# Kernel optimization log

Hardware: AMD Instinct MI355X
Metric: run time of the kernel (lower is better)

## Reference

```python
import jax, jax.numpy as jnp
import numpy as np

N, E = 50000, 800000
IN, HID, OUT = 256, 128, 128


def setup_inputs() -> dict:
    key = jax.random.key(0)
    ks = jax.random.split(key, 6)
    x = jax.random.normal(ks[0], (N, IN), dtype=jnp.float32)
    edge_index = jax.random.randint(ks[1], (2, E), 0, N, dtype=jnp.int32)
    # xavier_normal-ish scales (exact init values irrelevant for correctness baseline)
    W1 = jax.random.normal(ks[2], (IN, HID), dtype=jnp.float32) * (1.414 / np.sqrt(IN))
    att_src = jax.random.normal(ks[3], (HID,), dtype=jnp.float32) * 0.1
    att_dst = jax.random.normal(ks[4], (HID,), dtype=jnp.float32) * 0.1
    W2 = jax.random.normal(ks[5], (HID, OUT), dtype=jnp.float32) * (1.414 / np.sqrt(HID))
    return {"x": x, "edge_index": edge_index, "W1": W1,
            "att_src": att_src, "att_dst": att_dst, "W2": W2}


def _gat_layer(x, edge_index, W, a_src, a_dst):
    """GATConv(heads=1, concat=False, add_self_loops=False, dropout=0), attention=True."""
    n = x.shape[0]
    src, dst = edge_index[0], edge_index[1]  # message x_j = h[src], grouped by index = dst
    h = x @ W                                 # (N, C)
    e_src = h @ a_src                         # (N,) per-node attention logits
    e_dst = h @ a_dst                         # (N,)
    # per-edge: sigmoid(alpha_j + alpha_i), then scatter-softmax over dst neighborhoods
    alpha = jax.nn.sigmoid(e_src[src] + e_dst[dst])             # (E,)
    m = jax.ops.segment_max(alpha, dst, num_segments=n)          # stable softmax max
    ex = jnp.exp(alpha - m[dst])
    denom = jax.ops.segment_sum(ex, dst, num_segments=n)
    w = ex / denom[dst]                                          # (E,)
    # scatter-add aggregation of weighted source features; heads=1 so mean over heads is identity
    return jax.ops.segment_sum(h[src] * w[:, None], dst, num_segments=n)  # (N, C)


def reference(x, edge_index, W1, att_src, att_dst, W2):
    h1 = jax.nn.elu(_gat_layer(x, edge_index, W1, att_src, att_dst))
    # conv2 called with attention=False: mm(h1, W2).view(N,1,C).mean(1) == plain linear
    return h1 @ W2
```

## Files before the change

kernel.cpp:

```cpp
#include <hip/hip_runtime.h>
#include <hip/hip_bf16.h>

#define N_NODES 50000
#define N_EDGES 800000
#define DIN 256
#define DHID 128
#define DOUT 128
#define NBUCK 196
#define BINBLK 256
#define EPB 3125
#define BINIT 13
#define G1BLK ((N_NODES + 63) / 64)

typedef __attribute__((ext_vector_type(8))) short bf16x8;
typedef __attribute__((ext_vector_type(4))) float f32x4;

__device__ inline unsigned short f2b(float f) {
    __hip_bfloat16 b = __float2bfloat16(f);
    return *reinterpret_cast<unsigned short*>(&b);
}

__global__ __launch_bounds__(256) void convW_lhist_kernel(
    const float* __restrict__ W1, const float* __restrict__ W2,
    const int* __restrict__ ei,
    unsigned short* __restrict__ W1t, unsigned short* __restrict__ W2t,
    int* __restrict__ blockHist)
{
    __shared__ int h[NBUCK];
    const int blk = blockIdx.x;
    const int tid = threadIdx.x;

    if (blk < 192) {
        int i = blk * 256 + tid;
        if (i < DIN * DHID) {
            int n = i >> 8, k = i & 255;
            int kt = k >> 5, q = (k >> 3) & 3, e = k & 7;
            int t = n >> 4, m = n & 15;
            W1t[(((kt * 8 + t) * 64) + (q * 16 + m)) * 8 + e] = f2b(W1[k * DHID + n]);
        } else {
            int j = i - DIN * DHID;
            int n = j >> 7, k = j & 127;
            int kt = k >> 5, q = (k >> 3) & 3, e = k & 7;
            int t = n >> 4, m = n & 15;
            W2t[(((kt * 8 + t) * 64) + (q * 16 + m)) * 8 + e] = f2b(W2[k * DOUT + n]);
        }
        return;
    }

    const int b = blk - 192;
    if (tid < NBUCK) h[tid] = 0;
    __syncthreads();
    const int base = b * EPB;
    #pragma unroll 1
    for (int it = 0; it < BINIT; ++it) {
        int e = base + it * 256 + tid;
        if (e < base + EPB)
            atomicAdd(&h[ei[N_EDGES + e] >> 8], 1);
    }
    __syncthreads();
    if (tid < NBUCK) blockHist[tid * 256 + b] = h[tid];
}

__global__ __launch_bounds__(256) void gemm1_scan_kernel(
    const float* __restrict__ x,
    const unsigned short* __restrict__ W1t,
    const float* __restrict__ att_src,
    const float* __restrict__ att_dst,
    const int* __restrict__ blockHist,
    unsigned short* __restrict__ hb,
    float* __restrict__ es,
    float* __restrict__ ed,
    int* __restrict__ matrixScan)
{
    __shared__ unsigned short W1s[DHID * DIN];

    const int tid = threadIdx.x;

    if (blockIdx.x >= G1BLK) {
        int* bs = (int*)W1s;
        int* s  = bs + 256;
        const int b = blockIdx.x - G1BLK;

        int tot = 0;
        if (tid < NBUCK) {
            const int* row = blockHist + tid * 256;
            #pragma unroll 4
            for (int i = 0; i < 256; ++i) tot += row[i];
        }
        bs[tid] = tot;
        __syncthreads();
        #pragma unroll
        for (int off = 1; off < 256; off <<= 1) {
            int u = (tid >= off) ? bs[tid - off] : 0;
            __syncthreads();
            bs[tid] += u;
            __syncthreads();
        }
        const int base = (b == 0) ? 0 : bs[b - 1];

        int c = blockHist[b * 256 + tid];
        s[tid] = c;
        __syncthreads();
        #pragma unroll
        for (int off = 1; off < 256; off <<= 1) {
            int u = (tid >= off) ? s[tid - off] : 0;
            __syncthreads();
            s[tid] += u;
            __syncthreads();
        }
        matrixScan[b * 256 + tid] = base + s[tid] - c;
        return;
    }

    const int wave = tid >> 6, lane = tid & 63;
    const int row0 = blockIdx.x * 64 + wave * 16;
    const int m = lane & 15, q = lane >> 4;

    {
        const float4* src = (const float4*)W1t;
        float4* dst = (float4*)W1s;
        #pragma unroll
        for (int i = 0; i < 16; ++i)
            dst[tid + i * 256] = src[tid + i * 256];
    }
    __syncthreads();

    int r  = row0 + m;
    int rc = (r < N_NODES) ? r : 0;

    f32x4 acc[8];
    #pragma unroll
    for (int t = 0; t < 8; ++t) acc[t] = (f32x4){0.f, 0.f, 0.f, 0.f};

    const float* xr = x + (size_t)rc * DIN + q * 8;
    const short* wfrag = (const short*)W1s + lane * 8;

    #pragma unroll
    for (int kt = 0; kt < 8; ++kt) {
        float4 f0 = *(const float4*)(xr + kt * 32);
        float4 f1 = *(const float4*)(xr + kt * 32 + 4);
        bf16x8 a;
        a[0] = (short)f2b(f0.x); a[1] = (short)f2b(f0.y);
        a[2] = (short)f2b(f0.z); a[3] = (short)f2b(f0.w);
        a[4] = (short)f2b(f1.x); a[5] = (short)f2b(f1.y);
        a[6] = (short)f2b(f1.z); a[7] = (short)f2b(f1.w);
        #pragma unroll
        for (int t = 0; t < 8; ++t) {
            bf16x8 b = *(const bf16x8*)(wfrag + (kt * 8 + t) * 512);
            acc[t] = __builtin_amdgcn_mfma_f32_16x16x32_bf16(a, b, acc[t], 0, 0, 0);
        }
    }

    #pragma unroll
    for (int reg = 0; reg < 4; ++reg) {
        int rr = row0 + q * 4 + reg;
        if (rr < N_NODES) {
            #pragma unroll
            for (int t = 0; t < 8; ++t)
                hb[(size_t)rr * DHID + t * 16 + m] = f2b(acc[t][reg]);
        }
    }

    float esr[4] = {0.f, 0.f, 0.f, 0.f}, edr[4] = {0.f, 0.f, 0.f, 0.f};
    #pragma unroll
    for (int t = 0; t < 8; ++t) {
        float as = att_src[t * 16 + m];
        float ad = att_dst[t * 16 + m];
        #pragma unroll
        for (int reg = 0; reg < 4; ++reg) {
            esr[reg] += acc[t][reg] * as;
            edr[reg] += acc[t][reg] * ad;
        }
    }
    #pragma unroll
    for (int off = 8; off; off >>= 1)
        #pragma unroll
        for (int reg = 0; reg < 4; ++reg) {
            esr[reg] += __shfl_xor(esr[reg], off);
            edr[reg] += __shfl_xor(edr[reg], off);
        }
    if (m == 0) {
        #pragma unroll
        for (int reg = 0; reg < 4; ++reg) {
            int rr = row0 + q * 4 + reg;
            if (rr < N_NODES) { es[rr] = esr[reg]; ed[rr] = edr[reg]; }
        }
    }
}

__global__ __launch_bounds__(256) void binpass_kernel(
    const int* __restrict__ ei,
    const float* __restrict__ es,
    const float* __restrict__ ed,
    const int* __restrict__ matrixScan,
    int2* __restrict__ binned)
{
    __shared__ int lcur[NBUCK];
    const int t = threadIdx.x, blk = blockIdx.x;
    if (t < NBUCK) lcur[t] = matrixScan[t * 256 + blk];
    __syncthreads();
    const int base = blk * EPB;
    #pragma unroll 1
    for (int it = 0; it < BINIT; ++it) {
        int e = base + it * 256 + t;
        if (e < base + EPB) {
            int s = ei[e];
            int d = ei[N_EDGES + e];
            float a  = es[s] + ed[d];
            float sg = 1.f / (1.f + __expf(-a));
            float w  = __expf(sg);
            int pos = atomicAdd(&lcur[d >> 8], 1);
            binned[pos] = make_int2(s | ((d & 255) << 16), __float_as_int(w));
        }
    }
}

__global__ __launch_bounds__(256) void sortpass_kernel(
    const int2* __restrict__ binned,
    const int* __restrict__ matrixScan,
    int2* __restrict__ sortedSW,
    int* __restrict__ offset,
    int* __restrict__ count)
{
    __shared__ int lhist[256], lscan[256], lcur[256];
    const int t = threadIdx.x, b = blockIdx.x;
    const int start = matrixScan[b * 256];
    const int end   = (b == NBUCK - 1) ? N_EDGES : matrixScan[(b + 1) * 256];
    const int cnt   = end - start;

    lhist[t] = 0;
    __syncthreads();
    for (int i = t; i < cnt; i += 256)
        atomicAdd(&lhist[(binned[start + i].x >> 16) & 255], 1);
    __syncthreads();

    int v = lhist[t];
    lscan[t] = v;
    __syncthreads();
    #pragma unroll
    for (int off = 1; off < 256; off <<= 1) {
        int u = (t >= off) ? lscan[t - off] : 0;
        __syncthreads();
        lscan[t] += u;
        __syncthreads();
    }
    int excl = lscan[t] - v;

    int node = (b << 8) + t;
    if (node < N_NODES) { offset[node] = start + excl; count[node] = v; }
    lcur[t] = excl;
    __syncthreads();

    for (int i = t; i < cnt; i += 256) {
        int2 ent = binned[start + i];
        int dlow = (ent.x >> 16) & 255;
        int pos = atomicAdd(&lcur[dlow], 1);
        sortedSW[start + pos] = make_int2(ent.x & 0xFFFF, ent.y);
    }
}

__global__ __launch_bounds__(256) void agg_kernel(
    const int2* __restrict__ sortedSW,
    const int* __restrict__ offset,
    const int* __restrict__ count,
    const unsigned short* __restrict__ hb,
    unsigned int* __restrict__ h1b)
{
    int node = (blockIdx.x * 256 + threadIdx.x) >> 6;
    int lane = threadIdx.x & 63;
    if (node >= N_NODES) return;

    int beg = offset[node];
    int deg = count[node];

    float2 acc = make_float2(0.f, 0.f);
    float wsum = 0.f;

    for (int base = 0; base < deg; base += 64) {
        int cnt = min(64, deg - base);
        int2 sw = (lane < cnt) ? sortedSW[beg + base + lane] : make_int2(0, 0);
        int j = 0;

#define TIER(T)                                                                 \
        for (; j + T <= cnt; j += T) {                                          \
            unsigned uu[T]; float ww[T];                                        \
            _Pragma("unroll")                                                   \
            for (int k = 0; k < T; ++k) {                                       \
                int s_ = __builtin_amdgcn_readlane(sw.x, j + k);                \
                uu[k] = *(const unsigned*)(hb + (size_t)s_ * DHID + 2 * lane);  \
            }                                                                   \
            _Pragma("unroll")                                                   \
            for (int k = 0; k < T; ++k)                                         \
                ww[k] = __uint_as_float(                                        \
                    (unsigned)__builtin_amdgcn_readlane(sw.y, j + k));          \
            _Pragma("unroll")                                                   \
            for (int k = 0; k < T; ++k) {                                       \
                wsum  += ww[k];                                                 \
                acc.x += ww[k] * __uint_as_float(uu[k] << 16);                  \
                acc.y += ww[k] * __uint_as_float(uu[k] & 0xffff0000u);          \
            }                                                                   \
        }

        TIER(16)
        TIER(8)
        TIER(4)
#undef TIER
        for (; j < cnt; ++j) {
            int   sj = __builtin_amdgcn_readlane(sw.x, j);
            float wj = __uint_as_float((unsigned)__builtin_amdgcn_readlane(sw.y, j));
            unsigned u = *(const unsigned*)(hb + (size_t)sj * DHID + 2 * lane);
            acc.x += wj * __uint_as_float(u << 16);
            acc.y += wj * __uint_as_float(u & 0xffff0000u);
            wsum  += wj;
        }
    }
    float inv = (deg > 0) ? 1.f / wsum : 0.f;
    float v0 = acc.x * inv, v1 = acc.y * inv;
    float e0 = v0 > 0.f ? v0 : (__expf(v0) - 1.f);
    float e1 = v1 > 0.f ? v1 : (__expf(v1) - 1.f);
    h1b[(size_t)node * (DHID / 2) + lane] =
        (unsigned)f2b(e0) | ((unsigned)f2b(e1) << 16);
}

__global__ __launch_bounds__(256) void gemm2_mfma(
    const unsigned short* __restrict__ h1b,
    const unsigned short* __restrict__ W2t,
    float* __restrict__ out)
{
    __shared__ unsigned short W2s[DOUT * DHID];

    const int tid = threadIdx.x;
    const int wave = tid >> 6, lane = tid & 63;
    const int row0 = blockIdx.x * 64 + wave * 16;
    const int m = lane & 15, q = lane >> 4;

    {
        const float4* src = (const float4*)W2t;
        float4* dst = (float4*)W2s;
        #pragma unroll
        for (int i = 0; i < 8; ++i)
            dst[tid + i * 256] = src[tid + i * 256];
    }
    __syncthreads();

    int r  = row0 + m;
    int rc = (r < N_NODES) ? r : 0;

    f32x4 acc[8];
    #pragma unroll
    for (int t = 0; t < 8; ++t) acc[t] = (f32x4){0.f, 0.f, 0.f, 0.f};

    const short* xp = (const short*)h1b + (size_t)rc * DHID + q * 8;
    const short* wfrag = (const short*)W2s + lane * 8;

    #pragma unroll
    for (int kt = 0; kt < 4; ++kt) {
        bf16x8 a = *(const bf16x8*)(xp + kt * 32);
        #pragma unroll
        for (int t = 0; t < 8; ++t) {
            bf16x8 b = *(const bf16x8*)(wfrag + (kt * 8 + t) * 512);
            acc[t] = __builtin_amdgcn_mfma_f32_16x16x32_bf16(a, b, acc[t], 0, 0, 0);
        }
    }

    #pragma unroll
    for (int reg = 0; reg < 4; ++reg) {
        int rr = row0 + q * 4 + reg;
        if (rr < N_NODES) {
            #pragma unroll
            for (int t = 0; t < 8; ++t)
                out[(size_t)rr * DOUT + t * 16 + m] = acc[t][reg];
        }
    }
}

extern "C" void kernel_launch(void* const* d_in, const int* in_sizes, int n_in,
                              void* d_out, int out_size, void* d_ws, size_t ws_size,
                              hipStream_t stream)
{
    const float* x    = (const float*)d_in[0];
    const int*   ei   = (const int*)d_in[1];
    const float* W1   = (const float*)d_in[2];
    const float* asrc = (const float*)d_in[3];
    const float* adst = (const float*)d_in[4];
    const float* W2   = (const float*)d_in[5];
    float*       out  = (float*)d_out;

    char* p = (char*)d_ws;
    unsigned short* hb  = (unsigned short*)p;  p += (size_t)N_NODES * DHID * 2;
    unsigned int*   h1b = (unsigned int*)p;    p += (size_t)N_NODES * DHID * 2;
    unsigned short* W1t = (unsigned short*)p;  p += (size_t)DHID * DIN * 2;
    unsigned short* W2t = (unsigned short*)p;  p += (size_t)DOUT * DHID * 2;
    float* es     = (float*)p;  p += (size_t)N_NODES * 4;
    float* ed     = (float*)p;  p += (size_t)N_NODES * 4;
    int*   offset = (int*)p;    p += (size_t)N_NODES * 4;
    int*   count  = (int*)p;    p += (size_t)N_NODES * 4;
    int*   blockHist    = (int*)p; p += (size_t)NBUCK * 256 * 4;
    int*   matrixScan   = (int*)p; p += (size_t)NBUCK * 256 * 4;
    int2*  binned   = (int2*)p; p += (size_t)N_EDGES * 8;
    int2*  sortedSW = (int2*)p; p += (size_t)N_EDGES * 8;

    convW_lhist_kernel<<<192 + BINBLK, 256, 0, stream>>>(W1, W2, ei, W1t, W2t, blockHist);

    gemm1_scan_kernel<<<G1BLK + NBUCK, 256, 0, stream>>>(
        x, W1t, asrc, adst, blockHist, hb, es, ed, matrixScan);

    binpass_kernel  <<<BINBLK, 256, 0, stream>>>(ei, es, ed, matrixScan, binned);
    sortpass_kernel <<<NBUCK, 256, 0, stream>>>(binned, matrixScan, sortedSW, offset, count);
    agg_kernel<<<(N_NODES * 64 + 255) / 256, 256, 0, stream>>>(
        sortedSW, offset, count, hb, h1b);
    gemm2_mfma<<<G1BLK, 256, 0, stream>>>((const unsigned short*)h1b, W2t, out);
}
```

Measured before the change: 187.3 us.

## Drop LDS weight staging, double rows per wave, widen binning blocks to 1024

Both GEMMs now read the pre-swizzled bf16 weights directly from global/L2 instead of staging them in LDS, and each wave computes 32 rows with two accumulator sets that reuse each B fragment. The histogram, binning and sort kernels move to 1024-thread blocks with fewer loop iterations, and the 16-tier path in aggregation is removed. Removing the 64KB LDS staging should improve occupancy and cut per-block copy overhead, at the cost of more register pressure and uncached-in-LDS weight reads from L2.

```diff
diff --git a/kernel.cpp b/kernel.cpp
--- a/kernel.cpp
+++ b/kernel.cpp
@@ -9,8 +9,7 @@
 #define NBUCK 196
 #define BINBLK 256
 #define EPB 3125
-#define BINIT 13
-#define G1BLK ((N_NODES + 63) / 64)
+#define G1TILES 391
 
 typedef __attribute__((ext_vector_type(8))) short bf16x8;
 typedef __attribute__((ext_vector_type(4))) float f32x4;
@@ -20,7 +19,7 @@
     return *reinterpret_cast<unsigned short*>(&b);
 }
 
-__global__ __launch_bounds__(256) void convW_lhist_kernel(
+__global__ __launch_bounds__(1024) void convW_lhist_kernel(
     const float* __restrict__ W1, const float* __restrict__ W2,
     const int* __restrict__ ei,
     unsigned short* __restrict__ W1t, unsigned short* __restrict__ W2t,
@@ -30,8 +29,8 @@
     const int blk = blockIdx.x;
     const int tid = threadIdx.x;
 
-    if (blk < 192) {
-        int i = blk * 256 + tid;
+    if (blk < 48) {
+        int i = blk * 1024 + tid;
         if (i < DIN * DHID) {
             int n = i >> 8, k = i & 255;
             int kt = k >> 5, q = (k >> 3) & 3, e = k & 7;
@@ -47,13 +46,13 @@
         return;
     }
 
-    const int b = blk - 192;
+    const int b = blk - 48;
     if (tid < NBUCK) h[tid] = 0;
     __syncthreads();
     const int base = b * EPB;
     #pragma unroll 1
-    for (int it = 0; it < BINIT; ++it) {
-        int e = base + it * 256 + tid;
+    for (int it = 0; it < 4; ++it) {
+        int e = base + it * 1024 + tid;
         if (e < base + EPB)
             atomicAdd(&h[ei[N_EDGES + e] >> 8], 1);
     }
@@ -72,14 +71,12 @@
     float* __restrict__ ed,
     int* __restrict__ matrixScan)
 {
-    __shared__ unsigned short W1s[DHID * DIN];
-
+    __shared__ int bs[256];
+    __shared__ int sc[256];
     const int tid = threadIdx.x;
 
-    if (blockIdx.x >= G1BLK) {
-        int* bs = (int*)W1s;
-        int* s  = bs + 256;
-        const int b = blockIdx.x - G1BLK;
+    if (blockIdx.x >= G1TILES) {
+        const int b = blockIdx.x - G1TILES;
 
         int tot = 0;
         if (tid < NBUCK) {
@@ -99,96 +96,113 @@
         const int base = (b == 0) ? 0 : bs[b - 1];
 
         int c = blockHist[b * 256 + tid];
-        s[tid] = c;
+        sc[tid] = c;
         __syncthreads();
         #pragma unroll
         for (int off = 1; off < 256; off <<= 1) {
-            int u = (tid >= off) ? s[tid - off] : 0;
+            int u = (tid >= off) ? sc[tid - off] : 0;
             __syncthreads();
-            s[tid] += u;
+            sc[tid] += u;
             __syncthreads();
         }
-        matrixScan[b * 256 + tid] = base + s[tid] - c;
+        matrixScan[b * 256 + tid] = base + sc[tid] - c;
         return;
     }
 
     const int wave = tid >> 6, lane = tid & 63;
-    const int row0 = blockIdx.x * 64 + wave * 16;
+    const int row0 = blockIdx.x * 128 + wave * 32;
     const int m = lane & 15, q = lane >> 4;
 
-    {
-        const float4* src = (const float4*)W1t;
-        float4* dst = (float4*)W1s;
-        #pragma unroll
-        for (int i = 0; i < 16; ++i)
-            dst[tid + i * 256] = src[tid + i * 256];
-    }
-    __syncthreads();
-
-    int r  = row0 + m;
-    int rc = (r < N_NODES) ? r : 0;
-
-    f32x4 acc[8];
-    #pragma unroll
-    for (int t = 0; t < 8; ++t) acc[t] = (f32x4){0.f, 0.f, 0.f, 0.f};
-
-    const float* xr = x + (size_t)rc * DIN + q * 8;
-    const short* wfrag = (const short*)W1s + lane * 8;
+    int r0 = row0 + m;
+    int r1 = row0 + 16 + m;
+    int rc0 = (r0 < N_NODES) ? r0 : 0;
+    int rc1 = (r1 < N_NODES) ? r1 : 0;
+
+    f32x4 acc0[8], acc1[8];
+    #pragma unroll
+    for (int t = 0; t < 8; ++t) {
+        acc0[t] = (f32x4){0.f, 0.f, 0.f, 0.f};
+        acc1[t] = (f32x4){0.f, 0.f, 0.f, 0.f};
+    }
+
+    const float* xr0 = x + (size_t)rc0 * DIN + q * 8;
+    const float* xr1 = x + (size_t)rc1 * DIN + q * 8;
+    const short* wb  = (const short*)W1t + lane * 8;
 
     #pragma unroll
     for (int kt = 0; kt < 8; ++kt) {
-        float4 f0 = *(const float4*)(xr + kt * 32);
-        float4 f1 = *(const float4*)(xr + kt * 32 + 4);
-        bf16x8 a;
-        a[0] = (short)f2b(f0.x); a[1] = (short)f2b(f0.y);
-        a[2] = (short)f2b(f0.z); a[3] = (short)f2b(f0.w);
-        a[4] = (short)f2b(f1.x); a[5] = (short)f2b(f1.y);
-        a[6] = (short)f2b(f1.z); a[7] = (short)f2b(f1.w);
+        float4 f0 = *(const float4*)(xr0 + kt * 32);
+        float4 f1 = *(const float4*)(xr0 + kt * 32 + 4);
+        float4 g0 = *(const float4*)(xr1 + kt * 32);
+        float4 g1 = *(const float4*)(xr1 + kt * 32 + 4);
+        bf16x8 a0, a1;
+        a0[0] = (short)f2b(f0.x); a0[1] = (short)f2b(f0.y);
+        a0[2] = (short)f2b(f0.z); a0[3] = (short)f2b(f0.w);
+        a0[4] = (short)f2b(f1.x); a0[5] = (short)f2b(f1.y);
+        a0[6] = (short)f2b(f1.z); a0[7] = (short)f2b(f1.w);
+        a1[0] = (short)f2b(g0.x); a1[1] = (short)f2b(g0.y);
+        a1[2] = (short)f2b(g0.z); a1[3] = (short)f2b(g0.w);
+        a1[4] = (short)f2b(g1.x); a1[5] = (short)f2b(g1.y);
+        a1[6] = (short)f2b(g1.z); a1[7] = (short)f2b(g1.w);
         #pragma unroll
         for (int t = 0; t < 8; ++t) {
-            bf16x8 b = *(const bf16x8*)(wfrag + (kt * 8 + t) * 512);
-            acc[t] = __builtin_amdgcn_mfma_f32_16x16x32_bf16(a, b, acc[t], 0, 0, 0);
+            bf16x8 b = *(const bf16x8*)(wb + (kt * 8 + t) * 512);
+            acc0[t] = __builtin_amdgcn_mfma_f32_16x16x32_bf16(a0, b, acc0[t], 0, 0, 0);
+            acc1[t] = __builtin_amdgcn_mfma_f32_16x16x32_bf16(a1, b, acc1[t], 0, 0, 0);
         }
     }
 
     #pragma unroll
     for (int reg = 0; reg < 4; ++reg) {
-        int rr = row0 + q * 4 + reg;
-        if (rr < N_NODES) {
+        int ra = row0 + q * 4 + reg;
+        int rb = row0 + 16 + q * 4 + reg;
+        if (ra < N_NODES) {
             #pragma unroll
             for (int t = 0; t < 8; ++t)
-                hb[(size_t)rr * DHID + t * 16 + m] = f2b(acc[t][reg]);
-        }
-    }
-
-    float esr[4] = {0.f, 0.f, 0.f, 0.f}, edr[4] = {0.f, 0.f, 0.f, 0.f};
+                hb[(size_t)ra * DHID + t * 16 + m] = f2b(acc0[t][reg]);
+        }
+        if (rb < N_NODES) {
+            #pragma unroll
+            for (int t = 0; t < 8; ++t)
+                hb[(size_t)rb * DHID + t * 16 + m] = f2b(acc1[t][reg]);
+        }
+    }
+
+    float es0[4] = {0,0,0,0}, ed0[4] = {0,0,0,0};
+    float es1[4] = {0,0,0,0}, ed1[4] = {0,0,0,0};
     #pragma unroll
     for (int t = 0; t < 8; ++t) {
         float as = att_src[t * 16 + m];
         float ad = att_dst[t * 16 + m];
         #pragma unroll
         for (int reg = 0; reg < 4; ++reg) {
-            esr[reg] += acc[t][reg] * as;
-            edr[reg] += acc[t][reg] * ad;
+            es0[reg] += acc0[t][reg] * as;
+            ed0[reg] += acc0[t][reg] * ad;
+            es1[reg] += acc1[t][reg] * as;
+            ed1[reg] += acc1[t][reg] * ad;
         }
     }
     #pragma unroll
     for (int off = 8; off; off >>= 1)
         #pragma unroll
         for (int reg = 0; reg < 4; ++reg) {
-            esr[reg] += __shfl_xor(esr[reg], off);
-            edr[reg] += __shfl_xor(edr[reg], off);
+            es0[reg] += __shfl_xor(es0[reg], off);
+            ed0[reg] += __shfl_xor(ed0[reg], off);
+            es1[reg] += __shfl_xor(es1[reg], off);
+            ed1[reg] += __shfl_xor(ed1[reg], off);
         }
     if (m == 0) {
         #pragma unroll
         for (int reg = 0; reg < 4; ++reg) {
-            int rr = row0 + q * 4 + reg;
-            if (rr < N_NODES) { es[rr] = esr[reg]; ed[rr] = edr[reg]; }
-        }
-    }
-}
-
-__global__ __launch_bounds__(256) void binpass_kernel(
+            int ra = row0 + q * 4 + reg;
+            int rb = row0 + 16 + q * 4 + reg;
+            if (ra < N_NODES) { es[ra] = es0[reg]; ed[ra] = ed0[reg]; }
+            if (rb < N_NODES) { es[rb] = es1[reg]; ed[rb] = ed1[reg]; }
+        }
+    }
+}
+
+__global__ __launch_bounds__(1024) void binpass_kernel(
     const int* __restrict__ ei,
     const float* __restrict__ es,
     const float* __restrict__ ed,
@@ -201,8 +215,8 @@
     __syncthreads();
     const int base = blk * EPB;
     #pragma unroll 1
-    for (int it = 0; it < BINIT; ++it) {
-        int e = base + it * 256 + t;
+    for (int it = 0; it < 4; ++it) {
+        int e = base + it * 1024 + t;
         if (e < base + EPB) {
             int s = ei[e];
             int d = ei[N_EDGES + e];
@@ -215,7 +229,7 @@
     }
 }
 
-__global__ __launch_bounds__(256) void sortpass_kernel(
+__global__ __launch_bounds__(1024) void sortpass_kernel(
     const int2* __restrict__ binned,
     const int* __restrict__ matrixScan,
     int2* __restrict__ sortedSW,
@@ -228,30 +242,32 @@
     const int end   = (b == NBUCK - 1) ? N_EDGES : matrixScan[(b + 1) * 256];
     const int cnt   = end - start;
 
-    lhist[t] = 0;
-    __syncthreads();
-    for (int i = t; i < cnt; i += 256)
+    if (t < 256) lhist[t] = 0;
+    __syncthreads();
+    for (int i = t; i < cnt; i += 1024)
         atomicAdd(&lhist[(binned[start + i].x >> 16) & 255], 1);
     __syncthreads();
 
-    int v = lhist[t];
-    lscan[t] = v;
+    int v = 0;
+    if (t < 256) { v = lhist[t]; lscan[t] = v; }
     __syncthreads();
     #pragma unroll
     for (int off = 1; off < 256; off <<= 1) {
-        int u = (t >= off) ? lscan[t - off] : 0;
+        int u = 0;
+        if (t < 256 && t >= off) u = lscan[t - off];
         __syncthreads();
-        lscan[t] += u;
+        if (t < 256) lscan[t] += u;
         __syncthreads();
     }
-    int excl = lscan[t] - v;
-
-    int node = (b << 8) + t;
-    if (node < N_NODES) { offset[node] = start + excl; count[node] = v; }
-    lcur[t] = excl;
-    __syncthreads();
-
-    for (int i = t; i < cnt; i += 256) {
+    if (t < 256) {
+        int excl = lscan[t] - v;
+        int node = (b << 8) + t;
+        if (node < N_NODES) { offset[node] = start + excl; count[node] = v; }
+        lcur[t] = excl;
+    }
+    __syncthreads();
+
+    for (int i = t; i < cnt; i += 1024) {
         int2 ent = binned[start + i];
         int dlow = (ent.x >> 16) & 255;
         int pos = atomicAdd(&lcur[dlow], 1);
@@ -301,7 +317,6 @@
             }                                                                   \
         }
 
-        TIER(16)
         TIER(8)
         TIER(4)
 #undef TIER
@@ -327,49 +342,52 @@
     const unsigned short* __restrict__ W2t,
     float* __restrict__ out)
 {
-    __shared__ unsigned short W2s[DOUT * DHID];
-
     const int tid = threadIdx.x;
     const int wave = tid >> 6, lane = tid & 63;
-    const int row0 = blockIdx.x * 64 + wave * 16;
+    const int row0 = blockIdx.x * 128 + wave * 32;
     const int m = lane & 15, q = lane >> 4;
 
-    {
-        const float4* src = (const float4*)W2t;
-        float4* dst = (float4*)W2s;
-        #pragma unroll
-        for (int i = 0; i < 8; ++i)
-            dst[tid + i * 256] = src[tid + i * 256];
-    }
-    __syncthreads();
-
-    int r  = row0 + m;
-    int rc = (r < N_NODES) ? r : 0;
-
-    f32x4 acc[8];
-    #pragma unroll
-    for (int t = 0; t < 8; ++t) acc[t] = (f32x4){0.f, 0.f, 0.f, 0.f};
-
-    const short* xp = (const short*)h1b + (size_t)rc * DHID + q * 8;
-    const short* wfrag = (const short*)W2s + lane * 8;
+    int r0 = row0 + m;
+    int r1 = row0 + 16 + m;
+    int rc0 = (r0 < N_NODES) ? r0 : 0;
+    int rc1 = (r1 < N_NODES) ? r1 : 0;
+
+    f32x4 acc0[8], acc1[8];
+    #pragma unroll
+    for (int t = 0; t < 8; ++t) {
+        acc0[t] = (f32x4){0.f, 0.f, 0.f, 0.f};
+        acc1[t] = (f32x4){0.f, 0.f, 0.f, 0.f};
+    }
+
+    const short* xp0 = (const short*)h1b + (size_t)rc0 * DHID + q * 8;
+    const short* xp1 = (const short*)h1b + (size_t)rc1 * DHID + q * 8;
+    const short* wb  = (const short*)W2t + lane * 8;
 
     #pragma unroll
     for (int kt = 0; kt < 4; ++kt) {
-        bf16x8 a = *(const bf16x8*)(xp + kt * 32);
+        bf16x8 a0 = *(const bf16x8*)(xp0 + kt * 32);
+        bf16x8 a1 = *(const bf16x8*)(xp1 + kt * 32);
         #pragma unroll
         for (int t = 0; t < 8; ++t) {
-            bf16x8 b = *(const bf16x8*)(wfrag + (kt * 8 + t) * 512);
-            acc[t] = __builtin_amdgcn_mfma_f32_16x16x32_bf16(a, b, acc[t], 0, 0, 0);
+            bf16x8 b = *(const bf16x8*)(wb + (kt * 8 + t) * 512);
+            acc0[t] = __builtin_amdgcn_mfma_f32_16x16x32_bf16(a0, b, acc0[t], 0, 0, 0);
+            acc1[t] = __builtin_amdgcn_mfma_f32_16x16x32_bf16(a1, b, acc1[t], 0, 0, 0);
         }
     }
 
     #pragma unroll
     for (int reg = 0; reg < 4; ++reg) {
-        int rr = row0 + q * 4 + reg;
-        if (rr < N_NODES) {
+        int ra = row0 + q * 4 + reg;
+        int rb = row0 + 16 + q * 4 + reg;
+        if (ra < N_NODES) {
             #pragma unroll
             for (int t = 0; t < 8; ++t)
-                out[(size_t)rr * DOUT + t * 16 + m] = acc[t][reg];
+                out[(size_t)ra * DOUT + t * 16 + m] = acc0[t][reg];
+        }
+        if (rb < N_NODES) {
+            #pragma unroll
+            for (int t = 0; t < 8; ++t)
+                out[(size_t)rb * DOUT + t * 16 + m] = acc1[t][reg];
         }
     }
 }
@@ -400,14 +418,14 @@
     int2*  binned   = (int2*)p; p += (size_t)N_EDGES * 8;
     int2*  sortedSW = (int2*)p; p += (size_t)N_EDGES * 8;
 
-    convW_lhist_kernel<<<192 + BINBLK, 256, 0, stream>>>(W1, W2, ei, W1t, W2t, blockHist);
-
-    gemm1_scan_kernel<<<G1BLK + NBUCK, 256, 0, stream>>>(
+    convW_lhist_kernel<<<48 + BINBLK, 1024, 0, stream>>>(W1, W2, ei, W1t, W2t, blockHist);
+
+    gemm1_scan_kernel<<<G1TILES + NBUCK, 256, 0, stream>>>(
         x, W1t, asrc, adst, blockHist, hb, es, ed, matrixScan);
 
-    binpass_kernel  <<<BINBLK, 256, 0, stream>>>(ei, es, ed, matrixScan, binned);
-    sortpass_kernel <<<NBUCK, 256, 0, stream>>>(binned, matrixScan, sortedSW, offset, count);
+    binpass_kernel  <<<BINBLK, 1024, 0, stream>>>(ei, es, ed, matrixScan, binned);
+    sortpass_kernel <<<NBUCK, 1024, 0, stream>>>(binned, matrixScan, sortedSW, offset, count);
     agg_kernel<<<(N_NODES * 64 + 255) / 256, 256, 0, stream>>>(
         sortedSW, offset, count, hb, h1b);
-    gemm2_mfma<<<G1BLK, 256, 0, stream>>>((const unsigned short*)h1b, W2t, out);
-}
+    gemm2_mfma<<<G1TILES, 256, 0, stream>>>((const unsigned short*)h1b, W2t, out);
+}
```

Result: no change. 186.7 us (-0.3%).
